# Kernel optimization log

Hardware: AMD Instinct MI355X
Metric: run time of the kernel (lower is better)

The kernel has to match this reference:

```python
import jax, jax.numpy as jnp
import numpy as np

THETA = 10000.0


def rope_apply(x, pos, theta=THETA):
    # x: [..., S, d] with d even; rotates interleaved pairs (2k, 2k+1),
    # matching the block-diag 2x2 rotation matmul in the torch RoPE.
    d = x.shape[-1]
    half = d // 2
    inv_freq = 1.0 / (theta ** (2.0 * jnp.arange(half, dtype=jnp.float32) / d))
    ang = pos.astype(jnp.float32)[:, None] * inv_freq[None, :]  # [S, half]
    cos, sin = jnp.cos(ang), jnp.sin(ang)
    xe, xo = x[..., 0::2], x[..., 1::2]
    oe = cos * xe - sin * xo
    oo = sin * xe + cos * xo
    return jnp.stack([oe, oo], axis=-1).reshape(x.shape)


def setup_inputs() -> dict:
    key = jax.random.key(0)
    ks = jax.random.split(key, 5)
    B, S, D = 2, 2048, 1024
    scale = 0.02
    return {
        "x": jax.random.normal(ks[0], (B, S, D), dtype=jnp.float32),
        "token_positions": jnp.arange(S, dtype=jnp.int64 if jax.config.jax_enable_x64 else jnp.int32),
        "wq": jax.random.normal(ks[1], (D, D), dtype=jnp.float32) * scale,
        "wk": jax.random.normal(ks[2], (D, D), dtype=jnp.float32) * scale,
        "wv": jax.random.normal(ks[3], (D, D), dtype=jnp.float32) * scale,
        "wo": jax.random.normal(ks[4], (D, D), dtype=jnp.float32) * scale,
    }


def reference(x, token_positions, wq, wk, wv, wo):
    B, S, D = x.shape
    H = 16
    dk = D // H

    def split_heads(t):  # [B,S,D] -> [B,H,S,dk]
        return t.reshape(B, S, H, dk).swapaxes(1, 2)

    q = split_heads(jnp.einsum('bsd,ed->bse', x, wq))
    k = split_heads(jnp.einsum('bsd,ed->bse', x, wk))
    v = split_heads(jnp.einsum('bsd,ed->bse', x, wv))

    q = rope_apply(q, token_positions)
    k = rope_apply(k, token_positions)

    scores = jnp.einsum('bhqd,bhkd->bhqk', q, k) / jnp.sqrt(jnp.float32(dk))
    causal = jnp.tril(jnp.ones((S, S), dtype=bool))
    scores = jnp.where(causal, scores, -jnp.inf)
    p = jax.nn.softmax(scores, axis=-1)
    o = jnp.einsum('bhqk,bhkd->bhqd', p, v)          # [B,H,S,dk]
    o = o.swapaxes(1, 2).reshape(B, S, D)            # merge heads
    return jnp.einsum('bse,de->bsd', o, wo)          # out proj (wo.T)
```

## Files before the change

kernel.cpp:

```cpp
#include <hip/hip_runtime.h>

typedef unsigned short u16;
typedef __attribute__((ext_vector_type(8))) short short8;
typedef __attribute__((ext_vector_type(4))) float f32x4;

__device__ __forceinline__ u16 f2b(float f) {
  union { float f; unsigned u; } v; v.f = f;
  unsigned u = v.u;
  return (u16)((u + 0x7FFFu + ((u >> 16) & 1u)) >> 16);
}
__device__ __forceinline__ u16 f2b_trunc(float f) {
  union { float f; unsigned u; } v; v.f = f;
  return (u16)(v.u >> 16);
}
__device__ __forceinline__ float b2f(u16 h) {
  union { unsigned u; float f; } v; v.u = ((unsigned)h) << 16; return v.f;
}
__device__ __forceinline__ void glds16(const u16* g, u16* l) {
  __builtin_amdgcn_global_load_lds((const __attribute__((address_space(1))) void*)g,
                                   (__attribute__((address_space(3))) void*)l, 16, 0, 0);
}

__global__ __launch_bounds__(256) void f32_to_bf16_k(const float* __restrict__ src,
                                                     u16* __restrict__ dst, int n) {
  int i4 = (blockIdx.x * 256 + threadIdx.x) * 4;
  if (i4 >= n) return;
  const float4 v = *(const float4*)(src + i4);
  uint2 o;
  o.x = (unsigned)f2b(v.x) | ((unsigned)f2b(v.y) << 16);
  o.y = (unsigned)f2b(v.z) | ((unsigned)f2b(v.w) << 16);
  *(uint2*)(dst + i4) = o;
}

__global__ __launch_bounds__(256) void sincos_k(const int* __restrict__ pos,
                                                float* __restrict__ ct,
                                                float* __restrict__ st) {
  int idx = blockIdx.x * 256 + threadIdx.x;
  int i = idx & 31, s = idx >> 5;
  float p = (float)pos[s];
  float inv = expf(-(float)i * (logf(10000.0f) / 32.0f));
  float ang = p * inv;
  ct[idx] = cosf(ang);
  st[idx] = sinf(ang);
}

template <bool BF16OUT>
__global__ __launch_bounds__(256) void gemm_bt(const u16* __restrict__ A,
                                               const u16* __restrict__ B,
                                               void* __restrict__ Cv,
                                               int M, int N, int K) {
  __shared__ u16 As[128 * 32];
  __shared__ u16 Bs[128 * 32];
  const int tid = threadIdx.x;
  const int wv = tid >> 6, lane = tid & 63;
  const int quad = lane >> 4, l16 = lane & 15;
  const int wm = wv & 1, wn = wv >> 1;
  const int m0 = blockIdx.y * 128, n0 = blockIdx.x * 128;

  f32x4 acc[4][4];
  for (int i = 0; i < 4; i++)
    for (int j = 0; j < 4; j++) acc[i][j] = (f32x4){0.f, 0.f, 0.f, 0.f};

  for (int kt = 0; kt < K; kt += 32) {
    __syncthreads();
#pragma unroll
    for (int pass = 0; pass < 2; pass++) {
      int c = pass * 256 + tid;
      int row = c >> 2, k8 = c & 3;
      glds16(A + (size_t)(m0 + row) * K + kt + k8 * 8, As + (size_t)(c & ~63) * 8);
      glds16(B + (size_t)(n0 + row) * K + kt + k8 * 8, Bs + (size_t)(c & ~63) * 8);
    }
    __syncthreads();
    short8 af[4], bfr[4];
#pragma unroll
    for (int i = 0; i < 4; i++)
      af[i] = *(const short8*)(As + (wm * 64 + i * 16 + l16) * 32 + quad * 8);
#pragma unroll
    for (int j = 0; j < 4; j++)
      bfr[j] = *(const short8*)(Bs + (wn * 64 + j * 16 + l16) * 32 + quad * 8);
#pragma unroll
    for (int i = 0; i < 4; i++)
#pragma unroll
      for (int j = 0; j < 4; j++)
        acc[i][j] = __builtin_amdgcn_mfma_f32_16x16x32_bf16(af[i], bfr[j], acc[i][j], 0, 0, 0);
  }
  for (int i = 0; i < 4; i++)
    for (int j = 0; j < 4; j++) {
      int col = n0 + wn * 64 + j * 16 + l16;
      for (int r = 0; r < 4; r++) {
        int row = m0 + wm * 64 + i * 16 + quad * 4 + r;
        if (BF16OUT)
          ((u16*)Cv)[(size_t)row * N + col] = f2b(acc[i][j][r]);
        else
          ((float*)Cv)[(size_t)row * N + col] = acc[i][j][r];
      }
    }
}

__global__ __launch_bounds__(256) void repack_k(const u16* __restrict__ Cqkv,
                                                const float* __restrict__ ct,
                                                const float* __restrict__ st,
                                                u16* __restrict__ Qr,
                                                u16* __restrict__ Kr,
                                                u16* __restrict__ Vr) {
  int idx = blockIdx.x * 256 + threadIdx.x;
  int i = idx & 31;
  int h = (idx >> 5) & 15;
  int s = (idx >> 9) & 2047;
  int b = idx >> 20;
  size_t rowoff = (size_t)(b * 2048 + s) * 3072;
  int colq = h * 64 + 2 * i;
  unsigned qp = *(const unsigned*)(Cqkv + rowoff + colq);
  unsigned kp = *(const unsigned*)(Cqkv + rowoff + 1024 + colq);
  unsigned vp = *(const unsigned*)(Cqkv + rowoff + 2048 + colq);
  float qe = b2f((u16)qp), qo = b2f((u16)(qp >> 16));
  float ke = b2f((u16)kp), ko = b2f((u16)(kp >> 16));
  float c = ct[s * 32 + i], sn = st[s * 32 + i];
  float q0 = c * qe - sn * qo, q1 = sn * qe + c * qo;
  float k0 = c * ke - sn * ko, k1 = sn * ke + c * ko;
  size_t o = ((size_t)(b * 16 + h) * 2048 + s) * 64 + 2 * i;
  *(unsigned*)(Qr + o) = (unsigned)f2b(q0) | ((unsigned)f2b(q1) << 16);
  *(unsigned*)(Kr + o) = (unsigned)f2b(k0) | ((unsigned)f2b(k1) << 16);
  *(unsigned*)(Vr + o) = vp;
}

__global__ __launch_bounds__(256) void attn_k(const u16* __restrict__ Q,
                                              const u16* __restrict__ K,
                                              const u16* __restrict__ V,
                                              float* __restrict__ Op,
                                              float* __restrict__ Lp, int S) {
  __shared__ u16 Qs[8 * 512], Ks[8 * 512], Vt[8 * 520], Ps[8 * 520];
  const int tid = threadIdx.x;
  const int wv = tid >> 6, lane = tid & 63, quad = lane >> 4, l16 = lane & 15;
  const int bh = blockIdx.y, par = blockIdx.z;
  const u16* Qg = Q + (size_t)bh * S * 64;
  const u16* Kg = K + (size_t)bh * S * 64;
  const u16* Vg = V + (size_t)bh * S * 64;
  const int nqt = S >> 6;
  const float scale = 0.125f;
  const int rowbase = wv * 16 + quad * 4;
  float* Opb = Op + ((size_t)par * 32 + bh) * S * 64;
  float* Lpb = Lp + ((size_t)par * 32 + bh) * S;

  for (int t = 0; t < 2; t++) {
    const int qt = t ? (nqt - 1 - (int)blockIdx.x) : (int)blockIdx.x;
    const int q0 = qt * 64;
    for (int p = wv; p < 8; p += 4)
      glds16(Qg + (size_t)(q0 + lane) * 64 + p * 8, Qs + p * 512);
    __syncthreads();
    short8 qa0 = *(const short8*)(Qs + quad * 512 + (wv * 16 + l16) * 8);
    short8 qa1 = *(const short8*)(Qs + (4 + quad) * 512 + (wv * 16 + l16) * 8);

    f32x4 oacc[4];
    for (int j = 0; j < 4; j++) oacc[j] = (f32x4){0.f, 0.f, 0.f, 0.f};
    float l_r[4] = {0.f, 0.f, 0.f, 0.f};

    for (int kt = par; kt <= qt; kt += 2) {
      const int k0 = kt * 64;
      __syncthreads();
      for (int p = wv; p < 8; p += 4)
        glds16(Kg + (size_t)(k0 + lane) * 64 + p * 8, Ks + p * 512);
      for (int c = tid; c < 512; c += 256) {
        int sl = c >> 3, d8 = c & 7;
        int kp = sl >> 3, ko = sl & 7;
        u16 tmp[8];
        *(uint4*)tmp = *(const uint4*)(Vg + (size_t)(k0 + sl) * 64 + d8 * 8);
        int pl = kp ^ d8;
#pragma unroll
        for (int i = 0; i < 8; i++) Vt[pl * 520 + (d8 * 8 + i) * 8 + ko] = tmp[i];
      }
      __syncthreads();

      const bool diag = (kt == qt);
#pragma unroll
      for (int nt = 0; nt < 4; nt++) {
        f32x4 s4 = (f32x4){0.f, 0.f, 0.f, 0.f};
        short8 b0 = *(const short8*)(Ks + quad * 512 + (nt * 16 + l16) * 8);
        short8 b1 = *(const short8*)(Ks + (4 + quad) * 512 + (nt * 16 + l16) * 8);
        s4 = __builtin_amdgcn_mfma_f32_16x16x32_bf16(qa0, b0, s4, 0, 0, 0);
        s4 = __builtin_amdgcn_mfma_f32_16x16x32_bf16(qa1, b1, s4, 0, 0, 0);
        int col = nt * 16 + l16;
        int cp = col >> 3, co = col & 7;
#pragma unroll
        for (int r = 0; r < 4; r++) {
          float v = s4[r] * scale;
          v = fminf(v, 60.f);
          if (diag && col > rowbase + r) v = -1e30f;
          float p = __expf(v);
          l_r[r] += p;
          int row = rowbase + r;
          int A = (cp + 2 * (row >> 3)) & 7;
          Ps[A * 520 + row * 8 + co] = f2b_trunc(p);
        }
      }
      {
        int mr = wv * 16 + l16;
        int A0 = (quad + 2 * (mr >> 3)) & 7;
        short8 pa0 = *(const short8*)(Ps + A0 * 520 + mr * 8);
        short8 pa1 = *(const short8*)(Ps + ((A0 + 4) & 7) * 520 + mr * 8);
#pragma unroll
        for (int nt = 0; nt < 4; nt++) {
          int d = nt * 16 + l16, dh = d >> 3;
          int p0 = quad ^ dh;
          short8 vb0 = *(const short8*)(Vt + p0 * 520 + d * 8);
          short8 vb1 = *(const short8*)(Vt + (p0 ^ 4) * 520 + d * 8);
          oacc[nt] = __builtin_amdgcn_mfma_f32_16x16x32_bf16(pa0, vb0, oacc[nt], 0, 0, 0);
          oacc[nt] = __builtin_amdgcn_mfma_f32_16x16x32_bf16(pa1, vb1, oacc[nt], 0, 0, 0);
        }
      }
    }
#pragma unroll
    for (int r = 0; r < 4; r++) {
      l_r[r] += __shfl_xor(l_r[r], 1);
      l_r[r] += __shfl_xor(l_r[r], 2);
      l_r[r] += __shfl_xor(l_r[r], 4);
      l_r[r] += __shfl_xor(l_r[r], 8);
    }
    if (l16 == 0)
#pragma unroll
      for (int r = 0; r < 4; r++) Lpb[q0 + rowbase + r] = l_r[r];
#pragma unroll
    for (int nt = 0; nt < 4; nt++) {
      int col = nt * 16 + l16;
#pragma unroll
      for (int r = 0; r < 4; r++)
        Opb[(size_t)(q0 + rowbase + r) * 64 + col] = oacc[nt][r];
    }
    __syncthreads();
  }
}

__global__ __launch_bounds__(256) void combine_k(const float* __restrict__ Op,
                                                 const float* __restrict__ Lp,
                                                 u16* __restrict__ O, int S) {
  int idx = blockIdx.x * 256 + threadIdx.x;
  int d4 = idx & 15, s = (idx >> 4) & 2047, bh = idx >> 15;
  size_t po = (((size_t)bh * S) + s) * 64 + d4 * 4;
  size_t pstride = (size_t)32 * S * 64;
  float4 a = *(const float4*)(Op + po);
  float4 c = *(const float4*)(Op + pstride + po);
  float l = Lp[(size_t)bh * S + s] + Lp[(size_t)32 * S + (size_t)bh * S + s];
  float rl = 1.f / l;
  int b = bh >> 4, h = bh & 15;
  size_t oo = ((size_t)(b * S + s) * 16 + h) * 64 + d4 * 4;
  uint2 o;
  o.x = (unsigned)f2b((a.x + c.x) * rl) | ((unsigned)f2b((a.y + c.y) * rl) << 16);
  o.y = (unsigned)f2b((a.z + c.z) * rl) | ((unsigned)f2b((a.w + c.w) * rl) << 16);
  *(uint2*)(O + oo) = o;
}

extern "C" void kernel_launch(void* const* d_in, const int* in_sizes, int n_in,
                              void* d_out, int out_size, void* d_ws, size_t ws_size,
                              hipStream_t stream) {
  const float* x  = (const float*)d_in[0];
  const int*   tp = (const int*)d_in[1];
  const float* wq = (const float*)d_in[2];
  const float* wk = (const float*)d_in[3];
  const float* wvp = (const float*)d_in[4];
  const float* wo = (const float*)d_in[5];
  float* out = (float*)d_out;

  const int B = 2, S = 2048, D = 1024, H = 16;
  const int BS = B * S;

  char* ws = (char*)d_ws;
  u16*   xb    = (u16*)(ws);
  u16*   wqkvb = (u16*)(ws + ((size_t)8 << 20));
  u16*   wob   = (u16*)(ws + ((size_t)14 << 20));
  float* ct    = (float*)(ws + ((size_t)16 << 20));
  float* st    = (float*)(ws + ((size_t)16 << 20) + (256 << 10));
  u16*   cqkv  = (u16*)(ws + ((size_t)17 << 20));
  float* lpart = (float*)(ws + ((size_t)33 << 20));
  u16*   qr    = (u16*)(ws + ((size_t)41 << 20));
  u16*   ob    = (u16*)(ws + ((size_t)41 << 20));
  u16*   kr    = (u16*)(ws + ((size_t)49 << 20));
  u16*   vr    = (u16*)(ws + ((size_t)57 << 20));
  float* opart = (float*)(ws + ((size_t)65 << 20));

  f32_to_bf16_k<<<(BS * D) / 1024, 256, 0, stream>>>(x, xb, BS * D);
  f32_to_bf16_k<<<(D * D) / 1024, 256, 0, stream>>>(wq, wqkvb, D * D);
  f32_to_bf16_k<<<(D * D) / 1024, 256, 0, stream>>>(wk, wqkvb + D * D, D * D);
  f32_to_bf16_k<<<(D * D) / 1024, 256, 0, stream>>>(wvp, wqkvb + 2 * D * D, D * D);
  f32_to_bf16_k<<<(D * D) / 1024, 256, 0, stream>>>(wo, wob, D * D);
  sincos_k<<<(S * 32) / 256, 256, 0, stream>>>(tp, ct, st);

  dim3 g1(3 * D / 128, BS / 128);
  gemm_bt<true><<<g1, 256, 0, stream>>>(xb, wqkvb, cqkv, BS, 3 * D, D);

  repack_k<<<(B * S * H * 32) / 256, 256, 0, stream>>>(cqkv, ct, st, qr, kr, vr);

  dim3 ga(S / 128, B * H, 2);
  attn_k<<<ga, 256, 0, stream>>>(qr, kr, vr, opart, lpart, S);

  combine_k<<<(32 * S * 16) / 256, 256, 0, stream>>>(opart, lpart, ob, S);

  dim3 g2(D / 128, BS / 128);
  gemm_bt<false><<<g2, 256, 0, stream>>>(ob, wob, out, BS, D, D);
}
```

Measured before the change: 222.9 us.

## Fuse RoPE and head repack into QKV GEMM epilogue, store V transposed

Merges the five conversion launches and the sincos launch into one prep kernel. The QKV GEMM epilogue now applies RoPE through a lane shuffle and writes Q/K in head-major layout and V transposed, which removes the intermediate cqkv buffer and the separate repack kernel. Attention loads the pre-transposed V straight into LDS with async global-to-LDS copies and an XOR swizzle, replacing the per-element LDS transpose, and uses exp2 with a folded log2e scale. The price is scattered 2-byte global stores in the GEMM epilogue, especially the strided V-transpose writes.

```diff
diff --git a/kernel.cpp b/kernel.cpp
--- a/kernel.cpp
+++ b/kernel.cpp
@@ -13,42 +13,56 @@
   union { float f; unsigned u; } v; v.f = f;
   return (u16)(v.u >> 16);
 }
-__device__ __forceinline__ float b2f(u16 h) {
-  union { unsigned u; float f; } v; v.u = ((unsigned)h) << 16; return v.f;
-}
 __device__ __forceinline__ void glds16(const u16* g, u16* l) {
   __builtin_amdgcn_global_load_lds((const __attribute__((address_space(1))) void*)g,
                                    (__attribute__((address_space(3))) void*)l, 16, 0, 0);
 }
 
-__global__ __launch_bounds__(256) void f32_to_bf16_k(const float* __restrict__ src,
-                                                     u16* __restrict__ dst, int n) {
-  int i4 = (blockIdx.x * 256 + threadIdx.x) * 4;
-  if (i4 >= n) return;
-  const float4 v = *(const float4*)(src + i4);
-  uint2 o;
-  o.x = (unsigned)f2b(v.x) | ((unsigned)f2b(v.y) << 16);
-  o.y = (unsigned)f2b(v.z) | ((unsigned)f2b(v.w) << 16);
-  *(uint2*)(dst + i4) = o;
-}
-
-__global__ __launch_bounds__(256) void sincos_k(const int* __restrict__ pos,
-                                                float* __restrict__ ct,
-                                                float* __restrict__ st) {
-  int idx = blockIdx.x * 256 + threadIdx.x;
-  int i = idx & 31, s = idx >> 5;
-  float p = (float)pos[s];
-  float inv = expf(-(float)i * (logf(10000.0f) / 32.0f));
-  float ang = p * inv;
-  ct[idx] = cosf(ang);
-  st[idx] = sinf(ang);
-}
-
-template <bool BF16OUT>
-__global__ __launch_bounds__(256) void gemm_bt(const u16* __restrict__ A,
-                                               const u16* __restrict__ B,
-                                               void* __restrict__ Cv,
-                                               int M, int N, int K) {
+__global__ __launch_bounds__(256) void prep_k(const float* __restrict__ x,
+                                              const float* __restrict__ wq,
+                                              const float* __restrict__ wk,
+                                              const float* __restrict__ wv,
+                                              const float* __restrict__ wo,
+                                              const int* __restrict__ pos,
+                                              u16* __restrict__ xb,
+                                              u16* __restrict__ wqkvb,
+                                              u16* __restrict__ wob,
+                                              float* __restrict__ ct,
+                                              float* __restrict__ st) {
+  int bx = blockIdx.x, tid = threadIdx.x;
+  if (bx < 8192) {
+    const float* src; u16* dst; int base;
+    if (bx < 4096)      { src = x;  dst = xb;                base = bx; }
+    else if (bx < 5120) { src = wq; dst = wqkvb;             base = bx - 4096; }
+    else if (bx < 6144) { src = wk; dst = wqkvb + (1 << 20); base = bx - 5120; }
+    else if (bx < 7168) { src = wv; dst = wqkvb + (2 << 20); base = bx - 6144; }
+    else                { src = wo; dst = wob;               base = bx - 7168; }
+    int i4 = base * 1024 + tid * 4;
+    const float4 v = *(const float4*)(src + i4);
+    uint2 o;
+    o.x = (unsigned)f2b(v.x) | ((unsigned)f2b(v.y) << 16);
+    o.y = (unsigned)f2b(v.z) | ((unsigned)f2b(v.w) << 16);
+    *(uint2*)(dst + i4) = o;
+  } else {
+    int idx = (bx - 8192) * 256 + tid;
+    int i = idx & 31, s = idx >> 5;
+    float p = (float)pos[s];
+    float inv = expf(-(float)i * (logf(10000.0f) / 32.0f));
+    float ang = p * inv;
+    ct[idx] = cosf(ang);
+    st[idx] = sinf(ang);
+  }
+}
+
+__global__ __launch_bounds__(256) void gemm_qkv(const u16* __restrict__ A,
+                                                const u16* __restrict__ B,
+                                                const float* __restrict__ ct,
+                                                const float* __restrict__ st,
+                                                u16* __restrict__ Qr,
+                                                u16* __restrict__ Kr,
+                                                u16* __restrict__ VTg) {
+  const int M = 4096, N = 3072, K = 1024;
+  (void)M; (void)N;
   __shared__ u16 As[128 * 32];
   __shared__ u16 Bs[128 * 32];
   const int tid = threadIdx.x;
@@ -84,63 +98,110 @@
       for (int j = 0; j < 4; j++)
         acc[i][j] = __builtin_amdgcn_mfma_f32_16x16x32_bf16(af[i], bfr[j], acc[i][j], 0, 0, 0);
   }
+
+  const int region = n0 >> 10;
+  if (region < 2) {
+    u16* dst = region ? Kr : Qr;
+    const int par = l16 & 1;
+    for (int i = 0; i < 4; i++)
+      for (int j = 0; j < 4; j++) {
+        int col = n0 + wn * 64 + j * 16 + l16;
+        int cq = col & 1023;
+        int h = cq >> 6, d = cq & 63, ifr = (d >> 1) & 31;
+        for (int r = 0; r < 4; r++) {
+          int row = m0 + wm * 64 + i * 16 + quad * 4 + r;
+          int b = row >> 11, s = row & 2047;
+          float v = acc[i][j][r];
+          float vp = __shfl_xor(v, 1);
+          float c = ct[s * 32 + ifr], sn = st[s * 32 + ifr];
+          float o = par ? (sn * vp + c * v) : (c * v - sn * vp);
+          dst[((size_t)(b * 16 + h) * 2048 + s) * 64 + d] = f2b(o);
+        }
+      }
+  } else {
+    for (int i = 0; i < 4; i++)
+      for (int j = 0; j < 4; j++) {
+        int col = n0 + wn * 64 + j * 16 + l16;
+        int cq = col & 1023;
+        int h = cq >> 6, d = cq & 63;
+        for (int r = 0; r < 4; r++) {
+          int row = m0 + wm * 64 + i * 16 + quad * 4 + r;
+          int b = row >> 11, s = row & 2047;
+          VTg[((size_t)(b * 16 + h) * 64 + d) * 2048 + s] = f2b(acc[i][j][r]);
+        }
+      }
+  }
+}
+
+__global__ __launch_bounds__(256) void gemm_bt_f32(const u16* __restrict__ A,
+                                                   const u16* __restrict__ B,
+                                                   float* __restrict__ C,
+                                                   int M, int N, int K) {
+  __shared__ u16 As[128 * 32];
+  __shared__ u16 Bs[128 * 32];
+  const int tid = threadIdx.x;
+  const int wv = tid >> 6, lane = tid & 63;
+  const int quad = lane >> 4, l16 = lane & 15;
+  const int wm = wv & 1, wn = wv >> 1;
+  const int m0 = blockIdx.y * 128, n0 = blockIdx.x * 128;
+
+  f32x4 acc[4][4];
+  for (int i = 0; i < 4; i++)
+    for (int j = 0; j < 4; j++) acc[i][j] = (f32x4){0.f, 0.f, 0.f, 0.f};
+
+  for (int kt = 0; kt < K; kt += 32) {
+    __syncthreads();
+#pragma unroll
+    for (int pass = 0; pass < 2; pass++) {
+      int c = pass * 256 + tid;
+      int row = c >> 2, k8 = c & 3;
+      glds16(A + (size_t)(m0 + row) * K + kt + k8 * 8, As + (size_t)(c & ~63) * 8);
+      glds16(B + (size_t)(n0 + row) * K + kt + k8 * 8, Bs + (size_t)(c & ~63) * 8);
+    }
+    __syncthreads();
+    short8 af[4], bfr[4];
+#pragma unroll
+    for (int i = 0; i < 4; i++)
+      af[i] = *(const short8*)(As + (wm * 64 + i * 16 + l16) * 32 + quad * 8);
+#pragma unroll
+    for (int j = 0; j < 4; j++)
+      bfr[j] = *(const short8*)(Bs + (wn * 64 + j * 16 + l16) * 32 + quad * 8);
+#pragma unroll
+    for (int i = 0; i < 4; i++)
+#pragma unroll
+      for (int j = 0; j < 4; j++)
+        acc[i][j] = __builtin_amdgcn_mfma_f32_16x16x32_bf16(af[i], bfr[j], acc[i][j], 0, 0, 0);
+  }
   for (int i = 0; i < 4; i++)
     for (int j = 0; j < 4; j++) {
       int col = n0 + wn * 64 + j * 16 + l16;
       for (int r = 0; r < 4; r++) {
         int row = m0 + wm * 64 + i * 16 + quad * 4 + r;
-        if (BF16OUT)
-          ((u16*)Cv)[(size_t)row * N + col] = f2b(acc[i][j][r]);
-        else
-          ((float*)Cv)[(size_t)row * N + col] = acc[i][j][r];
-      }
-    }
-}
-
-__global__ __launch_bounds__(256) void repack_k(const u16* __restrict__ Cqkv,
-                                                const float* __restrict__ ct,
-                                                const float* __restrict__ st,
-                                                u16* __restrict__ Qr,
-                                                u16* __restrict__ Kr,
-                                                u16* __restrict__ Vr) {
-  int idx = blockIdx.x * 256 + threadIdx.x;
-  int i = idx & 31;
-  int h = (idx >> 5) & 15;
-  int s = (idx >> 9) & 2047;
-  int b = idx >> 20;
-  size_t rowoff = (size_t)(b * 2048 + s) * 3072;
-  int colq = h * 64 + 2 * i;
-  unsigned qp = *(const unsigned*)(Cqkv + rowoff + colq);
-  unsigned kp = *(const unsigned*)(Cqkv + rowoff + 1024 + colq);
-  unsigned vp = *(const unsigned*)(Cqkv + rowoff + 2048 + colq);
-  float qe = b2f((u16)qp), qo = b2f((u16)(qp >> 16));
-  float ke = b2f((u16)kp), ko = b2f((u16)(kp >> 16));
-  float c = ct[s * 32 + i], sn = st[s * 32 + i];
-  float q0 = c * qe - sn * qo, q1 = sn * qe + c * qo;
-  float k0 = c * ke - sn * ko, k1 = sn * ke + c * ko;
-  size_t o = ((size_t)(b * 16 + h) * 2048 + s) * 64 + 2 * i;
-  *(unsigned*)(Qr + o) = (unsigned)f2b(q0) | ((unsigned)f2b(q1) << 16);
-  *(unsigned*)(Kr + o) = (unsigned)f2b(k0) | ((unsigned)f2b(k1) << 16);
-  *(unsigned*)(Vr + o) = vp;
+        C[(size_t)row * N + col] = acc[i][j][r];
+      }
+    }
 }
 
 __global__ __launch_bounds__(256) void attn_k(const u16* __restrict__ Q,
                                               const u16* __restrict__ K,
-                                              const u16* __restrict__ V,
+                                              const u16* __restrict__ VT,
                                               float* __restrict__ Op,
                                               float* __restrict__ Lp, int S) {
-  __shared__ u16 Qs[8 * 512], Ks[8 * 512], Vt[8 * 520], Ps[8 * 520];
+  __shared__ u16 Qs[8 * 512], Ks[8 * 512], Vt[64 * 64], Ps[8 * 520];
   const int tid = threadIdx.x;
   const int wv = tid >> 6, lane = tid & 63, quad = lane >> 4, l16 = lane & 15;
   const int bh = blockIdx.y, par = blockIdx.z;
   const u16* Qg = Q + (size_t)bh * S * 64;
   const u16* Kg = K + (size_t)bh * S * 64;
-  const u16* Vg = V + (size_t)bh * S * 64;
+  const u16* Vg = VT + (size_t)bh * S * 64;
   const int nqt = S >> 6;
-  const float scale = 0.125f;
+  const float scale2 = 0.125f * 1.44269504f;
   const int rowbase = wv * 16 + quad * 4;
   float* Opb = Op + ((size_t)par * 32 + bh) * S * 64;
   float* Lpb = Lp + ((size_t)par * 32 + bh) * S;
+
+  const int vrow_off = lane >> 3;
+  const int vchunk = (lane & 7) ^ (lane >> 3);
 
   for (int t = 0; t < 2; t++) {
     const int qt = t ? (nqt - 1 - (int)blockIdx.x) : (int)blockIdx.x;
@@ -158,16 +219,9 @@
     for (int kt = par; kt <= qt; kt += 2) {
       const int k0 = kt * 64;
       __syncthreads();
-      for (int p = wv; p < 8; p += 4)
+      for (int p = wv; p < 8; p += 4) {
         glds16(Kg + (size_t)(k0 + lane) * 64 + p * 8, Ks + p * 512);
-      for (int c = tid; c < 512; c += 256) {
-        int sl = c >> 3, d8 = c & 7;
-        int kp = sl >> 3, ko = sl & 7;
-        u16 tmp[8];
-        *(uint4*)tmp = *(const uint4*)(Vg + (size_t)(k0 + sl) * 64 + d8 * 8);
-        int pl = kp ^ d8;
-#pragma unroll
-        for (int i = 0; i < 8; i++) Vt[pl * 520 + (d8 * 8 + i) * 8 + ko] = tmp[i];
+        glds16(Vg + (size_t)(p * 8 + vrow_off) * S + k0 + vchunk * 8, Vt + p * 512);
       }
       __syncthreads();
 
@@ -183,10 +237,10 @@
         int cp = col >> 3, co = col & 7;
 #pragma unroll
         for (int r = 0; r < 4; r++) {
-          float v = s4[r] * scale;
-          v = fminf(v, 60.f);
+          float v = s4[r] * scale2;
+          v = fminf(v, 86.f);
           if (diag && col > rowbase + r) v = -1e30f;
-          float p = __expf(v);
+          float p = exp2f(v);
           l_r[r] += p;
           int row = rowbase + r;
           int A = (cp + 2 * (row >> 3)) & 7;
@@ -198,12 +252,12 @@
         int A0 = (quad + 2 * (mr >> 3)) & 7;
         short8 pa0 = *(const short8*)(Ps + A0 * 520 + mr * 8);
         short8 pa1 = *(const short8*)(Ps + ((A0 + 4) & 7) * 520 + mr * 8);
+        int sl0 = quad ^ (l16 & 7);
 #pragma unroll
         for (int nt = 0; nt < 4; nt++) {
-          int d = nt * 16 + l16, dh = d >> 3;
-          int p0 = quad ^ dh;
-          short8 vb0 = *(const short8*)(Vt + p0 * 520 + d * 8);
-          short8 vb1 = *(const short8*)(Vt + (p0 ^ 4) * 520 + d * 8);
+          int d = nt * 16 + l16;
+          short8 vb0 = *(const short8*)(Vt + d * 64 + sl0 * 8);
+          short8 vb1 = *(const short8*)(Vt + d * 64 + (sl0 ^ 4) * 8);
           oacc[nt] = __builtin_amdgcn_mfma_f32_16x16x32_bf16(pa0, vb0, oacc[nt], 0, 0, 0);
           oacc[nt] = __builtin_amdgcn_mfma_f32_16x16x32_bf16(pa1, vb1, oacc[nt], 0, 0, 0);
         }
@@ -260,8 +314,9 @@
   const float* wo = (const float*)d_in[5];
   float* out = (float*)d_out;
 
-  const int B = 2, S = 2048, D = 1024, H = 16;
+  const int B = 2, S = 2048, D = 1024;
   const int BS = B * S;
+  (void)B; (void)D;
 
   char* ws = (char*)d_ws;
   u16*   xb    = (u16*)(ws);
@@ -269,31 +324,23 @@
   u16*   wob   = (u16*)(ws + ((size_t)14 << 20));
   float* ct    = (float*)(ws + ((size_t)16 << 20));
   float* st    = (float*)(ws + ((size_t)16 << 20) + (256 << 10));
-  u16*   cqkv  = (u16*)(ws + ((size_t)17 << 20));
-  float* lpart = (float*)(ws + ((size_t)33 << 20));
-  u16*   qr    = (u16*)(ws + ((size_t)41 << 20));
-  u16*   ob    = (u16*)(ws + ((size_t)41 << 20));
-  u16*   kr    = (u16*)(ws + ((size_t)49 << 20));
-  u16*   vr    = (u16*)(ws + ((size_t)57 << 20));
-  float* opart = (float*)(ws + ((size_t)65 << 20));
-
-  f32_to_bf16_k<<<(BS * D) / 1024, 256, 0, stream>>>(x, xb, BS * D);
-  f32_to_bf16_k<<<(D * D) / 1024, 256, 0, stream>>>(wq, wqkvb, D * D);
-  f32_to_bf16_k<<<(D * D) / 1024, 256, 0, stream>>>(wk, wqkvb + D * D, D * D);
-  f32_to_bf16_k<<<(D * D) / 1024, 256, 0, stream>>>(wvp, wqkvb + 2 * D * D, D * D);
-  f32_to_bf16_k<<<(D * D) / 1024, 256, 0, stream>>>(wo, wob, D * D);
-  sincos_k<<<(S * 32) / 256, 256, 0, stream>>>(tp, ct, st);
+  u16*   qr    = (u16*)(ws + ((size_t)17 << 20));
+  u16*   kr    = (u16*)(ws + ((size_t)25 << 20));
+  u16*   vtg   = (u16*)(ws + ((size_t)33 << 20));
+  float* lpart = (float*)(ws + ((size_t)41 << 20));
+  u16*   ob    = (u16*)(ws + ((size_t)42 << 20));
+  float* opart = (float*)(ws + ((size_t)50 << 20));
+
+  prep_k<<<8448, 256, 0, stream>>>(x, wq, wk, wvp, wo, tp, xb, wqkvb, wob, ct, st);
 
   dim3 g1(3 * D / 128, BS / 128);
-  gemm_bt<true><<<g1, 256, 0, stream>>>(xb, wqkvb, cqkv, BS, 3 * D, D);
-
-  repack_k<<<(B * S * H * 32) / 256, 256, 0, stream>>>(cqkv, ct, st, qr, kr, vr);
-
-  dim3 ga(S / 128, B * H, 2);
-  attn_k<<<ga, 256, 0, stream>>>(qr, kr, vr, opart, lpart, S);
+  gemm_qkv<<<g1, 256, 0, stream>>>(xb, wqkvb, ct, st, qr, kr, vtg);
+
+  dim3 ga(S / 128, 32, 2);
+  attn_k<<<ga, 256, 0, stream>>>(qr, kr, vtg, opart, lpart, S);
 
   combine_k<<<(32 * S * 16) / 256, 256, 0, stream>>>(opart, lpart, ob, S);
 
   dim3 g2(D / 128, BS / 128);
-  gemm_bt<false><<<g2, 256, 0, stream>>>(ob, wob, out, BS, D, D);
-}
+  gemm_bt_f32<<<g2, 256, 0, stream>>>(ob, wob, out, BS, D, D);
+}
```

Result: faster. 216.2 us (-3.0%).
